# Optimization experiments

Hardware: AMD Instinct MI355X
Metric: run time of the kernel (lower is better)

## Reference

```python
import jax, jax.numpy as jnp
import numpy as np

B, T, E, H, OUT = 64, 2048, 512, 32, 131


def setup_inputs() -> dict:
    key = jax.random.key(0)
    ks = jax.random.split(key, 12)
    x = jax.random.normal(ks[0], (B, T, E), dtype=jnp.float32)
    # pack_padded_sequence(enforce_sorted=True) requires descending lengths
    src_len = jnp.sort(jax.random.randint(ks[1], (B,), 1, T + 1))[::-1]
    other_input = jax.random.normal(ks[2], (B, OUT), dtype=jnp.float32)
    s_ih, s_hh = 1.0 / np.sqrt(E), 1.0 / np.sqrt(H)
    W_ih_f = jax.random.normal(ks[3], (3 * H, E), dtype=jnp.float32) * s_ih
    W_hh_f = jax.random.normal(ks[4], (3 * H, H), dtype=jnp.float32) * s_hh
    b_ih_f = jax.random.normal(ks[5], (3 * H,), dtype=jnp.float32) * s_hh
    b_hh_f = jax.random.normal(ks[6], (3 * H,), dtype=jnp.float32) * s_hh
    W_ih_b = jax.random.normal(ks[7], (3 * H, E), dtype=jnp.float32) * s_ih
    W_hh_b = jax.random.normal(ks[8], (3 * H, H), dtype=jnp.float32) * s_hh
    b_ih_b = jax.random.normal(ks[9], (3 * H,), dtype=jnp.float32) * s_hh
    b_hh_b = jax.random.normal(ks[10], (3 * H,), dtype=jnp.float32) * s_hh
    fc_W = jax.random.normal(ks[11], (OUT, 2 * H), dtype=jnp.float32) * (1.0 / np.sqrt(2 * H))
    fc_b = jnp.zeros((OUT,), dtype=jnp.float32)
    return {"x": x, "src_len": src_len, "other_input": other_input,
            "W_ih_f": W_ih_f, "W_hh_f": W_hh_f, "b_ih_f": b_ih_f, "b_hh_f": b_hh_f,
            "W_ih_b": W_ih_b, "W_hh_b": W_hh_b, "b_ih_b": b_ih_b, "b_hh_b": b_hh_b,
            "fc_W": fc_W, "fc_b": fc_b}


def _gru_dir(x_proj, W_hh, b_hh, lengths, reverse):
    # x_proj: [B,T,3H] precomputed input gates; mask updates where t < length
    xs = jnp.swapaxes(x_proj, 0, 1)  # [T,B,3H]
    ts = jnp.arange(xs.shape[0])
    if reverse:
        xs, ts = xs[::-1], ts[::-1]

    def step(h, inp):
        gx, t = inp
        gh = h @ W_hh.T + b_hh
        xr, xz, xn = jnp.split(gx, 3, axis=-1)
        hr, hz, hn = jnp.split(gh, 3, axis=-1)
        r = jax.nn.sigmoid(xr + hr)
        z = jax.nn.sigmoid(xz + hz)
        n = jnp.tanh(xn + r * hn)
        h_new = (1.0 - z) * n + z * h
        mask = (t < lengths)[:, None]
        return jnp.where(mask, h_new, h), None

    h0 = jnp.zeros((x_proj.shape[0], W_hh.shape[1]), dtype=x_proj.dtype)
    h, _ = jax.lax.scan(step, h0, (xs, ts))
    return h  # [B,H] final hidden of this direction


def reference(x, src_len, other_input, W_ih_f, W_hh_f, b_ih_f, b_hh_f,
              W_ih_b, W_hh_b, b_ih_b, b_hh_b, fc_W, fc_b):
    lengths = src_len.astype(jnp.int32)
    # batched input projections (the only big GEMMs)
    xp_f = jnp.einsum('bte,ge->btg', x, W_ih_f) + b_ih_f  # [B,T,3H]
    xp_b = jnp.einsum('bte,ge->btg', x, W_ih_b) + b_ih_b
    h_f = _gru_dir(xp_f, W_hh_f, b_hh_f, lengths, reverse=False)
    h_b = _gru_dir(xp_b, W_hh_b, b_hh_b, lengths, reverse=True)
    # hidden_state[-2]=fwd, hidden_state[-1]=bwd for 1-layer bidirectional GRU
    hidden = jnp.concatenate([h_f, h_b], axis=1)  # [B,2H]
    return hidden @ fc_W.T + fc_b  # [B,OUT]
```

## Files before the change

kernel.cpp:

```cpp
#include <hip/hip_runtime.h>
#include <hip/hip_bf16.h>
#include <cstddef>
#include <cstdint>

typedef __bf16 bf16_t;
typedef __fp16 fp16_t;
typedef __attribute__((ext_vector_type(2))) __fp16 h16x2;
typedef __attribute__((ext_vector_type(8))) __bf16 bf16x8;
typedef __attribute__((ext_vector_type(4))) float f32x4;
typedef __attribute__((ext_vector_type(2))) unsigned u32x2;

#define B_  64
#define T_  2048
#define E_  512
#define H_  32
#define G_  96
#define N2_ 192
#define OUT_ 131

#define C1_ (-1.44269504088896340736f)
#define C2_ ( 2.88539008177792681472f)

#define MOVDPP(out_, in_, N_)                                               \
    asm("v_mov_b32_dpp %0, %1 row_ror:" #N_ " row_mask:0xf bank_mask:0xf"   \
        : "=v"(out_) : "v"(in_))

__global__ void prep_kernel(const float* __restrict__ Wf, const float* __restrict__ Wb,
                            const float* __restrict__ bf_, const float* __restrict__ bb_,
                            const float* __restrict__ bhf, const float* __restrict__ bhb,
                            bf16_t* __restrict__ Wbf, float* __restrict__ bias) {
    int idx = blockIdx.x * 256 + threadIdx.x;
    int g = idx >> 9, k = idx & 511;
    float v = (g < G_) ? Wf[g * E_ + k] : Wb[(g - G_) * E_ + k];
    Wbf[idx] = (bf16_t)v;
    if (idx < N2_) {
        int dn = (idx >= G_) ? 1 : 0;
        int lg = idx - G_ * dn;
        const float* bi = dn ? bb_ : bf_;
        const float* bh = dn ? bhb : bhf;
        bias[idx] = bi[lg] + ((lg < 64) ? bh[lg] : 0.0f);
    }
}

__global__ __launch_bounds__(256) void proj_kernel(
    const float* __restrict__ x,
    const bf16_t* __restrict__ Wbf,
    const float* __restrict__ bias,
    const int*   __restrict__ srcl,
    float* __restrict__ xp4)
{
    __shared__ bf16_t Alds[64][72];
    __shared__ bf16_t Blds[96][72];

    const int tid  = threadIdx.x;
    const int lane = tid & 63;
    const int w    = tid >> 6;
    const int wm   = w & 1;
    const int wn   = w >> 1;
    const int m0   = blockIdx.y * 64;
    const int n0   = blockIdx.x * 96;

    const int arow = tid >> 2;
    const int acol = (tid & 3) * 16;

    f32x4 acc[2][3];
    #pragma unroll
    for (int i = 0; i < 2; ++i)
        #pragma unroll
        for (int jn = 0; jn < 3; ++jn)
            acc[i][jn] = (f32x4){0.f, 0.f, 0.f, 0.f};

    for (int kt = 0; kt < 8; ++kt) {
        const int c0 = kt * 64;
        __syncthreads();
        {
            const float* asrc = x + (size_t)(m0 + arow) * E_ + c0 + acol;
            float4 v0 = *(const float4*)(asrc + 0);
            float4 v1 = *(const float4*)(asrc + 4);
            float4 v2 = *(const float4*)(asrc + 8);
            float4 v3 = *(const float4*)(asrc + 12);
            bf16x8 pa, pb;
            pa[0]=(bf16_t)v0.x; pa[1]=(bf16_t)v0.y; pa[2]=(bf16_t)v0.z; pa[3]=(bf16_t)v0.w;
            pa[4]=(bf16_t)v1.x; pa[5]=(bf16_t)v1.y; pa[6]=(bf16_t)v1.z; pa[7]=(bf16_t)v1.w;
            pb[0]=(bf16_t)v2.x; pb[1]=(bf16_t)v2.y; pb[2]=(bf16_t)v2.z; pb[3]=(bf16_t)v2.w;
            pb[4]=(bf16_t)v3.x; pb[5]=(bf16_t)v3.y; pb[6]=(bf16_t)v3.z; pb[7]=(bf16_t)v3.w;
            *(bf16x8*)&Alds[arow][acol]     = pa;
            *(bf16x8*)&Alds[arow][acol + 8] = pb;
        }
        #pragma unroll
        for (int i = 0; i < 3; ++i) {
            int u = tid + i * 256;
            int brow = u >> 3, koff = (u & 7) * 8;
            bf16x8 bv = *(const bf16x8*)(Wbf + (size_t)(n0 + brow) * E_ + c0 + koff);
            *(bf16x8*)&Blds[brow][koff] = bv;
        }
        __syncthreads();
        #pragma unroll
        for (int ks = 0; ks < 2; ++ks) {
            bf16x8 af[2], bfr[3];
            #pragma unroll
            for (int i = 0; i < 2; ++i)
                af[i] = *(const bf16x8*)&Alds[wm * 32 + i * 16 + (lane & 15)][ks * 32 + (lane >> 4) * 8];
            #pragma unroll
            for (int jn = 0; jn < 3; ++jn)
                bfr[jn] = *(const bf16x8*)&Blds[wn * 48 + jn * 16 + (lane & 15)][ks * 32 + (lane >> 4) * 8];
            #pragma unroll
            for (int i = 0; i < 2; ++i)
                #pragma unroll
                for (int jn = 0; jn < 3; ++jn)
                    acc[i][jn] = __builtin_amdgcn_mfma_f32_16x16x32_bf16(af[i], bfr[jn], acc[i][jn], 0, 0, 0);
        }
    }
    const int bb = m0 >> 11;
    int len = srcl[bb];
    if (len < 1) len = 1;
    if (len > T_) len = T_;
    float* xb4 = xp4 + (size_t)bb * 512 * N2_ * 4;
    #pragma unroll
    for (int i = 0; i < 2; ++i)
        #pragma unroll
        for (int jn = 0; jn < 3; ++jn) {
            int mg = m0 + wm * 32 + i * 16 + ((lane >> 4) & 3) * 4;
            int ng = n0 + wn * 48 + jn * 16 + (lane & 15);
            int lg = (ng >= G_) ? ng - G_ : ng;
            float scl = (lg < 64) ? C1_ : C2_;
            float bv  = bias[ng];
            int t = mg & (T_ - 1);
            if (ng < G_) {
                f32x4 v;
                #pragma unroll
                for (int r = 0; r < 4; ++r) v[r] = scl * (acc[i][jn][r] + bv);
                *(f32x4*)(xb4 + ((size_t)(t >> 2) * N2_ + ng) * 4) = v;
            } else {
                #pragma unroll
                for (int r = 0; r < 4; ++r) {
                    int trow = len - 1 - (t + r);
                    if (trow < 0) trow += T_;
                    xb4[((size_t)(trow >> 2) * N2_ + ng) * 4 + (trow & 3)] =
                        scl * (acc[i][jn][r] + bv);
                }
            }
        }
}

__global__ __launch_bounds__(64) void gru_rec_kernel(
    const float* __restrict__ xp4,
    const int*   __restrict__ src_len,
    const float* __restrict__ Whh_f, const float* __restrict__ bhh_f,
    const float* __restrict__ Whh_b, const float* __restrict__ bhh_b,
    float* __restrict__ hout)
{
    const int b    = blockIdx.x;
    const int l    = threadIdx.x;
    const int m    = l & 15;
    const int r16  = (l >> 4) & 1;
    const int dir  = l >> 5;
    const int j    = l & 31;

    const float* Whh = dir ? Whh_b : Whh_f;
    const float* bhh = dir ? bhh_b : bhh_f;

    int s_dir;
    {
        int q1;
        MOVDPP(q1, m, 1);
        s_dir = (__builtin_amdgcn_readfirstlane(q1) == 1) ? 1 : -1;
    }

    h16x2 wr[16], wz[16], wn[16];
    #pragma unroll
    for (int i = 0; i < 16; ++i) {
        int c  = (m + s_dir * i) & 15;
        int ka = c + 16 * r16;
        int kb = c + 16 * (1 - r16);
        wr[i] = (h16x2){(fp16_t)(C1_ * Whh[(j)      * H_ + ka]), (fp16_t)(C1_ * Whh[(j)      * H_ + kb])};
        wz[i] = (h16x2){(fp16_t)(C1_ * Whh[(32 + j) * H_ + ka]), (fp16_t)(C1_ * Whh[(32 + j) * H_ + kb])};
        wn[i] = (h16x2){(fp16_t)(C2_ * Whh[(64 + j) * H_ + ka]), (fp16_t)(C2_ * Whh[(64 + j) * H_ + kb])};
    }
    const float bn = C2_ * bhh[64 + j];

#if __has_builtin(__builtin_amdgcn_permlane16_swap)
    bool useX;
    {
        u32x2 pr = __builtin_amdgcn_permlane16_swap((unsigned)l, (unsigned)l, false, false);
        useX = (pr.x == (unsigned)(l ^ 16));
    }
#endif

    int len = src_len[b];
    if (len < 1) len = 1;
    if (len > T_) len = T_;
    len = __builtin_amdgcn_readfirstlane(len);

    const int off = dir * G_ + j;
    const float* xb4 = xp4 + (size_t)b * 512 * N2_ * 4;

    float hval = 0.0f;

    auto LB = [&](int q4, f32x4& vr, f32x4& vz, f32x4& vn) {
        int qq = (q4 < 512) ? q4 : 511;
        const f32x4* p = (const f32x4*)(xb4 + ((size_t)qq * N2_ + off) * 4);
        vr = p[0]; vz = p[32]; vn = p[64];
    };

    auto step = [&](float xr, float xz, float xn) {
        float hB;
#if __has_builtin(__builtin_amdgcn_permlane16_swap)
        {
            u32x2 sw = __builtin_amdgcn_permlane16_swap(
                __float_as_uint(hval), __float_as_uint(hval), false, false);
            hB = __uint_as_float(useX ? sw.x : sw.y);
        }
#else
        hB = __int_as_float(__builtin_amdgcn_ds_bpermute((l ^ 16) << 2, __float_as_int(hval)));
#endif
        auto q0 = __builtin_amdgcn_cvt_pkrtz(hval, hB);
        int qb = __builtin_bit_cast(int, q0);
        float ar = xr, az = xz, an = bn;
        {
            h16x2 p0 = __builtin_bit_cast(h16x2, qb);
            ar = __builtin_amdgcn_fdot2(p0, wr[0], ar, false);
            az = __builtin_amdgcn_fdot2(p0, wz[0], az, false);
            an = __builtin_amdgcn_fdot2(p0, wn[0], an, false);
        }
#define DOTI(N_)                                                    \
        {   int rb_;                                                \
            MOVDPP(rb_, qb, N_);                                    \
            h16x2 p_ = __builtin_bit_cast(h16x2, rb_);              \
            ar = __builtin_amdgcn_fdot2(p_, wr[N_], ar, false);     \
            az = __builtin_amdgcn_fdot2(p_, wz[N_], az, false);     \
            an = __builtin_amdgcn_fdot2(p_, wn[N_], an, false);     }
        DOTI(1)  DOTI(2)  DOTI(3)  DOTI(4)  DOTI(5)
        DOTI(6)  DOTI(7)  DOTI(8)  DOTI(9)  DOTI(10)
        DOTI(11) DOTI(12) DOTI(13) DOTI(14) DOTI(15)
#undef DOTI
        float er = __builtin_amdgcn_exp2f(ar);
        float rg = __builtin_amdgcn_rcpf(1.0f + er);
        float ez = __builtin_amdgcn_exp2f(az);
        float zg = __builtin_amdgcn_rcpf(1.0f + ez);
        float na = __builtin_fmaf(rg, an, xn);
        float eu = __builtin_amdgcn_exp2f(na);
        float u  = __builtin_amdgcn_rcpf(1.0f + eu);
        float m2 = -(ez + ez);
        float hp = hval + ez;
        hval = zg * __builtin_fmaf(m2, u, hp);
    };

    f32x4 Ar, Az, An, Cr, Cz, Cn;
    LB(0, Ar, Az, An);
    LB(1, Cr, Cz, Cn);
    int s = 0;
    while (s + 8 <= len) {
        step(Ar[0], Az[0], An[0]);
        step(Ar[1], Az[1], An[1]);
        step(Ar[2], Az[2], An[2]);
        step(Ar[3], Az[3], An[3]);
        LB((s >> 2) + 2, Ar, Az, An);
        step(Cr[0], Cz[0], Cn[0]);
        step(Cr[1], Cz[1], Cn[1]);
        step(Cr[2], Cz[2], Cn[2]);
        step(Cr[3], Cz[3], Cn[3]);
        LB((s >> 2) + 3, Cr, Cz, Cn);
        s += 8;
    }
    #pragma unroll
    for (int d = 0; d < 4; ++d)
        if (s + d < len) step(Ar[d], Az[d], An[d]);
    #pragma unroll
    for (int d = 0; d < 4; ++d)
        if (s + 4 + d < len) step(Cr[d], Cz[d], Cn[d]);

    hout[b * 64 + dir * 32 + j] = hval;
}

__global__ __launch_bounds__(192) void fc_kernel(
    const float* __restrict__ hbuf,
    const float* __restrict__ fcW,
    const float* __restrict__ fcb,
    float* __restrict__ out)
{
    __shared__ float hrow[64];
    const int b = blockIdx.x, tid = threadIdx.x;
    if (tid < 64) hrow[tid] = hbuf[b * 64 + tid];
    __syncthreads();
    if (tid < OUT_) {
        float acc = fcb[tid];
        #pragma unroll
        for (int i = 0; i < 64; ++i)
            acc = __builtin_fmaf(hrow[i], fcW[tid * 64 + i], acc);
        out[b * OUT_ + tid] = acc;
    }
}

extern "C" void kernel_launch(void* const* d_in, const int* in_sizes, int n_in,
                              void* d_out, int out_size, void* d_ws, size_t ws_size,
                              hipStream_t stream) {
    const float* x    = (const float*)d_in[0];
    const int*   srcl = (const int*)  d_in[1];
    const float* Wihf = (const float*)d_in[3];
    const float* Whhf = (const float*)d_in[4];
    const float* bihf = (const float*)d_in[5];
    const float* bhhf = (const float*)d_in[6];
    const float* Wihb = (const float*)d_in[7];
    const float* Whhb = (const float*)d_in[8];
    const float* bihb = (const float*)d_in[9];
    const float* bhhb = (const float*)d_in[10];
    const float* fcW  = (const float*)d_in[11];
    const float* fcb  = (const float*)d_in[12];
    float* out = (float*)d_out;

    const size_t XP_BYTES   = (size_t)B_ * T_ * N2_ * 4;
    const size_t HBUF_BYTES = (size_t)B_ * 64 * 4;
    const size_t BIAS_BYTES = 1024;
    const size_t WBF_BYTES  = (size_t)N2_ * E_ * 2;
    if (ws_size < XP_BYTES + HBUF_BYTES + BIAS_BYTES + WBF_BYTES) return;

    char* ws = (char*)d_ws;
    float*  xp4  = (float*)ws;
    float*  hbuf = (float*)(ws + XP_BYTES);
    float*  bias = (float*)(ws + XP_BYTES + HBUF_BYTES);
    bf16_t* Wbf  = (bf16_t*)(ws + XP_BYTES + HBUF_BYTES + BIAS_BYTES);

    prep_kernel<<<384, 256, 0, stream>>>(Wihf, Wihb, bihf, bihb, bhhf, bhhb, Wbf, bias);
    dim3 pg(2, (B_ * T_) / 64);
    proj_kernel<<<pg, 256, 0, stream>>>(x, Wbf, bias, srcl, xp4);
    gru_rec_kernel<<<B_, 64, 0, stream>>>(xp4, srcl, Whhf, bhhf, Whhb, bhhb, hbuf);
    fc_kernel<<<B_, 192, 0, stream>>>(hbuf, fcW, fcb, out);
}
```

Baseline: 454.8 us.

## Fuse projection GEMM and GRU recurrence with per-batch completion counters

```diff
diff --git a/kernel.cpp b/kernel.cpp
--- a/kernel.cpp
+++ b/kernel.cpp
@@ -28,7 +28,8 @@
 __global__ void prep_kernel(const float* __restrict__ Wf, const float* __restrict__ Wb,
                             const float* __restrict__ bf_, const float* __restrict__ bb_,
                             const float* __restrict__ bhf, const float* __restrict__ bhb,
-                            bf16_t* __restrict__ Wbf, float* __restrict__ bias) {
+                            bf16_t* __restrict__ Wbf, float* __restrict__ bias,
+                            int* __restrict__ done) {
     int idx = blockIdx.x * 256 + threadIdx.x;
     int g = idx >> 9, k = idx & 511;
     float v = (g < G_) ? Wf[g * E_ + k] : Wb[(g - G_) * E_ + k];
@@ -40,118 +41,129 @@
         const float* bh = dn ? bhb : bhf;
         bias[idx] = bi[lg] + ((lg < 64) ? bh[lg] : 0.0f);
     }
+    if (idx < B_) done[idx] = 0;
 }
 
-__global__ __launch_bounds__(256) void proj_kernel(
-    const float* __restrict__ x,
-    const bf16_t* __restrict__ Wbf,
-    const float* __restrict__ bias,
-    const int*   __restrict__ srcl,
-    float* __restrict__ xp4)
+__global__ __launch_bounds__(256) void fused_kernel(
+    const float* x,
+    const bf16_t* Wbf,
+    const float* bias,
+    const int* src_len,
+    const float* Whh_f, const float* bhh_f,
+    const float* Whh_b, const float* bhh_b,
+    float* xp4,
+    float* hout,
+    int* done)
 {
     __shared__ bf16_t Alds[64][72];
     __shared__ bf16_t Blds[96][72];
 
-    const int tid  = threadIdx.x;
-    const int lane = tid & 63;
-    const int w    = tid >> 6;
-    const int wm   = w & 1;
-    const int wn   = w >> 1;
-    const int m0   = blockIdx.y * 64;
-    const int n0   = blockIdx.x * 96;
-
-    const int arow = tid >> 2;
-    const int acol = (tid & 3) * 16;
-
-    f32x4 acc[2][3];
-    #pragma unroll
-    for (int i = 0; i < 2; ++i)
+    if (blockIdx.x >= 64) {
+        const int bx   = blockIdx.x - 64;
+        const int tid  = threadIdx.x;
+        const int lane = tid & 63;
+        const int w    = tid >> 6;
+        const int wm   = w & 1;
+        const int wn   = w >> 1;
+        const int m0   = (bx >> 1) * 64;
+        const int n0   = (bx & 1) * 96;
+
+        const int arow = tid >> 2;
+        const int acol = (tid & 3) * 16;
+
+        f32x4 acc[2][3];
         #pragma unroll
-        for (int jn = 0; jn < 3; ++jn)
-            acc[i][jn] = (f32x4){0.f, 0.f, 0.f, 0.f};
-
-    for (int kt = 0; kt < 8; ++kt) {
-        const int c0 = kt * 64;
-        __syncthreads();
-        {
-            const float* asrc = x + (size_t)(m0 + arow) * E_ + c0 + acol;
-            float4 v0 = *(const float4*)(asrc + 0);
-            float4 v1 = *(const float4*)(asrc + 4);
-            float4 v2 = *(const float4*)(asrc + 8);
-            float4 v3 = *(const float4*)(asrc + 12);
-            bf16x8 pa, pb;
-            pa[0]=(bf16_t)v0.x; pa[1]=(bf16_t)v0.y; pa[2]=(bf16_t)v0.z; pa[3]=(bf16_t)v0.w;
-            pa[4]=(bf16_t)v1.x; pa[5]=(bf16_t)v1.y; pa[6]=(bf16_t)v1.z; pa[7]=(bf16_t)v1.w;
-            pb[0]=(bf16_t)v2.x; pb[1]=(bf16_t)v2.y; pb[2]=(bf16_t)v2.z; pb[3]=(bf16_t)v2.w;
-            pb[4]=(bf16_t)v3.x; pb[5]=(bf16_t)v3.y; pb[6]=(bf16_t)v3.z; pb[7]=(bf16_t)v3.w;
-            *(bf16x8*)&Alds[arow][acol]     = pa;
-            *(bf16x8*)&Alds[arow][acol + 8] = pb;
-        }
-        #pragma unroll
-        for (int i = 0; i < 3; ++i) {
-            int u = tid + i * 256;
-            int brow = u >> 3, koff = (u & 7) * 8;
-            bf16x8 bv = *(const bf16x8*)(Wbf + (size_t)(n0 + brow) * E_ + c0 + koff);
-            *(bf16x8*)&Blds[brow][koff] = bv;
-        }
-        __syncthreads();
-        #pragma unroll
-        for (int ks = 0; ks < 2; ++ks) {
-            bf16x8 af[2], bfr[3];
-            #pragma unroll
-            for (int i = 0; i < 2; ++i)
-                af[i] = *(const bf16x8*)&Alds[wm * 32 + i * 16 + (lane & 15)][ks * 32 + (lane >> 4) * 8];
+        for (int i = 0; i < 2; ++i)
             #pragma unroll
             for (int jn = 0; jn < 3; ++jn)
-                bfr[jn] = *(const bf16x8*)&Blds[wn * 48 + jn * 16 + (lane & 15)][ks * 32 + (lane >> 4) * 8];
+                acc[i][jn] = (f32x4){0.f, 0.f, 0.f, 0.f};
+
+        for (int kt = 0; kt < 8; ++kt) {
+            const int c0 = kt * 64;
+            __syncthreads();
+            {
+                const float* asrc = x + (size_t)(m0 + arow) * E_ + c0 + acol;
+                float4 v0 = *(const float4*)(asrc + 0);
+                float4 v1 = *(const float4*)(asrc + 4);
+                float4 v2 = *(const float4*)(asrc + 8);
+                float4 v3 = *(const float4*)(asrc + 12);
+                bf16x8 pa, pb;
+                pa[0]=(bf16_t)v0.x; pa[1]=(bf16_t)v0.y; pa[2]=(bf16_t)v0.z; pa[3]=(bf16_t)v0.w;
+                pa[4]=(bf16_t)v1.x; pa[5]=(bf16_t)v1.y; pa[6]=(bf16_t)v1.z; pa[7]=(bf16_t)v1.w;
+                pb[0]=(bf16_t)v2.x; pb[1]=(bf16_t)v2.y; pb[2]=(bf16_t)v2.z; pb[3]=(bf16_t)v2.w;
+                pb[4]=(bf16_t)v3.x; pb[5]=(bf16_t)v3.y; pb[6]=(bf16_t)v3.z; pb[7]=(bf16_t)v3.w;
+                *(bf16x8*)&Alds[arow][acol]     = pa;
+                *(bf16x8*)&Alds[arow][acol + 8] = pb;
+            }
             #pragma unroll
-            for (int i = 0; i < 2; ++i)
+            for (int i = 0; i < 3; ++i) {
+                int u = tid + i * 256;
+                int brow = u >> 3, koff = (u & 7) * 8;
+                bf16x8 bv = *(const bf16x8*)(Wbf + (size_t)(n0 + brow) * E_ + c0 + koff);
+                *(bf16x8*)&Blds[brow][koff] = bv;
+            }
+            __syncthreads();
+            #pragma unroll
+            for (int ks = 0; ks < 2; ++ks) {
+                bf16x8 af[2], bfr[3];
+                #pragma unroll
+                for (int i = 0; i < 2; ++i)
+                    af[i] = *(const bf16x8*)&Alds[wm * 32 + i * 16 + (lane & 15)][ks * 32 + (lane >> 4) * 8];
                 #pragma unroll
                 for (int jn = 0; jn < 3; ++jn)
-                    acc[i][jn] = __builtin_amdgcn_mfma_f32_16x16x32_bf16(af[i], bfr[jn], acc[i][jn], 0, 0, 0);
+                    bfr[jn] = *(const bf16x8*)&Blds[wn * 48 + jn * 16 + (lane & 15)][ks * 32 + (lane >> 4) * 8];
+                #pragma unroll
+                for (int i = 0; i < 2; ++i)
+                    #pragma unroll
+                    for (int jn = 0; jn < 3; ++jn)
+                        acc[i][jn] = __builtin_amdgcn_mfma_f32_16x16x32_bf16(af[i], bfr[jn], acc[i][jn], 0, 0, 0);
+            }
         }
-    }
-    const int bb = m0 >> 11;
-    int len = srcl[bb];
-    if (len < 1) len = 1;
-    if (len > T_) len = T_;
-    float* xb4 = xp4 + (size_t)bb * 512 * N2_ * 4;
-    #pragma unroll
-    for (int i = 0; i < 2; ++i)
+        const int bb = m0 >> 11;
+        int len = src_len[bb];
+        if (len < 1) len = 1;
+        if (len > T_) len = T_;
+        float* xb4 = xp4 + (size_t)bb * 512 * N2_ * 4;
         #pragma unroll
-        for (int jn = 0; jn < 3; ++jn) {
-            int mg = m0 + wm * 32 + i * 16 + ((lane >> 4) & 3) * 4;
-            int ng = n0 + wn * 48 + jn * 16 + (lane & 15);
-            int lg = (ng >= G_) ? ng - G_ : ng;
-            float scl = (lg < 64) ? C1_ : C2_;
-            float bv  = bias[ng];
-            int t = mg & (T_ - 1);
-            if (ng < G_) {
-                f32x4 v;
-                #pragma unroll
-                for (int r = 0; r < 4; ++r) v[r] = scl * (acc[i][jn][r] + bv);
-                *(f32x4*)(xb4 + ((size_t)(t >> 2) * N2_ + ng) * 4) = v;
-            } else {
-                #pragma unroll
-                for (int r = 0; r < 4; ++r) {
-                    int trow = len - 1 - (t + r);
-                    if (trow < 0) trow += T_;
-                    xb4[((size_t)(trow >> 2) * N2_ + ng) * 4 + (trow & 3)] =
-                        scl * (acc[i][jn][r] + bv);
+        for (int i = 0; i < 2; ++i)
+            #pragma unroll
+            for (int jn = 0; jn < 3; ++jn) {
+                int mg = m0 + wm * 32 + i * 16 + ((lane >> 4) & 3) * 4;
+                int ng = n0 + wn * 48 + jn * 16 + (lane & 15);
+                int lg = (ng >= G_) ? ng - G_ : ng;
+                float scl = (lg < 64) ? C1_ : C2_;
+                float bv  = bias[ng];
+                int t = mg & (T_ - 1);
+                if (ng < G_) {
+                    f32x4 v;
+                    #pragma unroll
+                    for (int r = 0; r < 4; ++r) v[r] = scl * (acc[i][jn][r] + bv);
+                    *(f32x4*)(xb4 + ((size_t)(t >> 2) * N2_ + ng) * 4) = v;
+                } else {
+                    #pragma unroll
+                    for (int r = 0; r < 4; ++r) {
+                        int trow = len - 1 - (t + r);
+                        if (trow < 0) trow += T_;
+                        xb4[((size_t)(trow >> 2) * N2_ + ng) * 4 + (trow & 3)] =
+                            scl * (acc[i][jn][r] + bv);
+                    }
                 }
             }
-        }
-}
-
-__global__ __launch_bounds__(64) void gru_rec_kernel(
-    const float* __restrict__ xp4,
-    const int*   __restrict__ src_len,
-    const float* __restrict__ Whh_f, const float* __restrict__ bhh_f,
-    const float* __restrict__ Whh_b, const float* __restrict__ bhh_b,
-    float* __restrict__ hout)
-{
-    const int b    = blockIdx.x;
-    const int l    = threadIdx.x;
+        __threadfence();
+        __syncthreads();
+        if (tid == 0) atomicAdd(&done[bb], 1);
+        return;
+    }
+
+    const int b = blockIdx.x;
+    const int l = threadIdx.x;
+    if (l >= 64) return;
+
+    if (l == 0) {
+        while (atomicAdd(&done[b], 0) < 64) {}
+    }
+    __threadfence();
+
     const int m    = l & 15;
     const int r16  = (l >> 4) & 1;
     const int dir  = l >> 5;
@@ -313,17 +325,18 @@
     const size_t HBUF_BYTES = (size_t)B_ * 64 * 4;
     const size_t BIAS_BYTES = 1024;
     const size_t WBF_BYTES  = (size_t)N2_ * E_ * 2;
-    if (ws_size < XP_BYTES + HBUF_BYTES + BIAS_BYTES + WBF_BYTES) return;
+    const size_t DONE_BYTES = 256;
+    if (ws_size < XP_BYTES + HBUF_BYTES + BIAS_BYTES + WBF_BYTES + DONE_BYTES) return;
 
     char* ws = (char*)d_ws;
     float*  xp4  = (float*)ws;
     float*  hbuf = (float*)(ws + XP_BYTES);
     float*  bias = (float*)(ws + XP_BYTES + HBUF_BYTES);
     bf16_t* Wbf  = (bf16_t*)(ws + XP_BYTES + HBUF_BYTES + BIAS_BYTES);
-
-    prep_kernel<<<384, 256, 0, stream>>>(Wihf, Wihb, bihf, bihb, bhhf, bhhb, Wbf, bias);
-    dim3 pg(2, (B_ * T_) / 64);
-    proj_kernel<<<pg, 256, 0, stream>>>(x, Wbf, bias, srcl, xp4);
-    gru_rec_kernel<<<B_, 64, 0, stream>>>(xp4, srcl, Whhf, bhhf, Whhb, bhhb, hbuf);
+    int*    done = (int*)(ws + XP_BYTES + HBUF_BYTES + BIAS_BYTES + WBF_BYTES);
+
+    prep_kernel<<<384, 256, 0, stream>>>(Wihf, Wihb, bihf, bihb, bhhf, bhhb, Wbf, bias, done);
+    fused_kernel<<<64 + (B_ * T_) / 64 * 2, 256, 0, stream>>>(
+        x, Wbf, bias, srcl, Whhf, bhhf, Whhb, bhhb, xp4, hbuf, done);
     fc_kernel<<<B_, 192, 0, stream>>>(hbuf, fcW, fcb, out);
 }
```

Result: slower. 1.045 ms (+129.7%).

## Split GRU recurrence across two half-waves per direction with permlane32 reduction

Applied to the files above, without the earlier changes.

```diff
diff --git a/kernel.cpp b/kernel.cpp
--- a/kernel.cpp
+++ b/kernel.cpp
@@ -21,9 +21,13 @@
 #define C1_ (-1.44269504088896340736f)
 #define C2_ ( 2.88539008177792681472f)
 
-#define MOVDPP(out_, in_, N_)                                               \
-    asm("v_mov_b32_dpp %0, %1 row_ror:" #N_ " row_mask:0xf bank_mask:0xf"   \
-        : "=v"(out_) : "v"(in_))
+#if __has_builtin(__builtin_amdgcn_mov_dpp)
+#define DPPROT(out_, in_, N_) (out_) = __builtin_amdgcn_mov_dpp((in_), 0x120 + (N_), 0xf, 0xf, false)
+#else
+#define DPPROT(out_, in_, N_)                                               \
+    asm("s_nop 1\n\ts_nop 1\n\tv_mov_b32_dpp %0, %1 row_ror:" #N_           \
+        " row_mask:0xf bank_mask:0xf" : "=v"(out_) : "v"(in_))
+#endif
 
 __global__ void prep_kernel(const float* __restrict__ Wf, const float* __restrict__ Wb,
                             const float* __restrict__ bf_, const float* __restrict__ bb_,
@@ -150,11 +154,13 @@
     const float* __restrict__ Whh_b, const float* __restrict__ bhh_b,
     float* __restrict__ hout)
 {
-    const int b    = blockIdx.x;
+    const int blk  = blockIdx.x;
+    const int b    = blk >> 1;
+    const int dir  = blk & 1;
     const int l    = threadIdx.x;
     const int m    = l & 15;
     const int r16  = (l >> 4) & 1;
-    const int dir  = l >> 5;
+    const int p32  = l >> 5;
     const int j    = l & 31;
 
     const float* Whh = dir ? Whh_b : Whh_f;
@@ -163,21 +169,21 @@
     int s_dir;
     {
         int q1;
-        MOVDPP(q1, m, 1);
+        DPPROT(q1, m, 1);
         s_dir = (__builtin_amdgcn_readfirstlane(q1) == 1) ? 1 : -1;
     }
 
-    h16x2 wr[16], wz[16], wn[16];
-    #pragma unroll
-    for (int i = 0; i < 16; ++i) {
-        int c  = (m + s_dir * i) & 15;
+    h16x2 wr[8], wz[8], wn[8];
+    #pragma unroll
+    for (int i = 0; i < 8; ++i) {
+        int c  = (m + s_dir * (i + 8 * p32)) & 15;
         int ka = c + 16 * r16;
         int kb = c + 16 * (1 - r16);
         wr[i] = (h16x2){(fp16_t)(C1_ * Whh[(j)      * H_ + ka]), (fp16_t)(C1_ * Whh[(j)      * H_ + kb])};
         wz[i] = (h16x2){(fp16_t)(C1_ * Whh[(32 + j) * H_ + ka]), (fp16_t)(C1_ * Whh[(32 + j) * H_ + kb])};
         wn[i] = (h16x2){(fp16_t)(C2_ * Whh[(64 + j) * H_ + ka]), (fp16_t)(C2_ * Whh[(64 + j) * H_ + kb])};
     }
-    const float bn = C2_ * bhh[64 + j];
+    const float bnseed = p32 ? 0.0f : (C2_ * bhh[64 + j]);
 
 #if __has_builtin(__builtin_amdgcn_permlane16_swap)
     bool useX;
@@ -199,8 +205,17 @@
 
     auto LB = [&](int q4, f32x4& vr, f32x4& vz, f32x4& vn) {
         int qq = (q4 < 512) ? q4 : 511;
-        const f32x4* p = (const f32x4*)(xb4 + ((size_t)qq * N2_ + off) * 4);
-        vr = p[0]; vz = p[32]; vn = p[64];
+        const f32x4* pp = (const f32x4*)(xb4 + ((size_t)qq * N2_ + off) * 4);
+        vr = pp[0]; vz = pp[32]; vn = pp[64];
+    };
+
+    auto pl32sum = [&](float a) -> float {
+#if __has_builtin(__builtin_amdgcn_permlane32_swap)
+        u32x2 rr = __builtin_amdgcn_permlane32_swap(__float_as_uint(a), __float_as_uint(a), false, false);
+        return __uint_as_float(rr.x) + __uint_as_float(rr.y);
+#else
+        return a + __int_as_float(__builtin_amdgcn_ds_bpermute((l ^ 32) << 2, __float_as_int(a)));
+#endif
     };
 
     auto step = [&](float xr, float xz, float xn) {
@@ -216,29 +231,33 @@
 #endif
         auto q0 = __builtin_amdgcn_cvt_pkrtz(hval, hB);
         int qb = __builtin_bit_cast(int, q0);
-        float ar = xr, az = xz, an = bn;
+        int qb8;
+        DPPROT(qb8, qb, 8);
+        int qc = p32 ? qb8 : qb;
+        float ar = 0.f, az = 0.f, an = bnseed;
         {
-            h16x2 p0 = __builtin_bit_cast(h16x2, qb);
-            ar = __builtin_amdgcn_fdot2(p0, wr[0], ar, false);
-            az = __builtin_amdgcn_fdot2(p0, wz[0], az, false);
-            an = __builtin_amdgcn_fdot2(p0, wn[0], an, false);
+            h16x2 p_ = __builtin_bit_cast(h16x2, qc);
+            ar = __builtin_amdgcn_fdot2(p_, wr[0], ar, false);
+            az = __builtin_amdgcn_fdot2(p_, wz[0], az, false);
+            an = __builtin_amdgcn_fdot2(p_, wn[0], an, false);
         }
 #define DOTI(N_)                                                    \
         {   int rb_;                                                \
-            MOVDPP(rb_, qb, N_);                                    \
+            DPPROT(rb_, qc, N_);                                    \
             h16x2 p_ = __builtin_bit_cast(h16x2, rb_);              \
             ar = __builtin_amdgcn_fdot2(p_, wr[N_], ar, false);     \
             az = __builtin_amdgcn_fdot2(p_, wz[N_], az, false);     \
             an = __builtin_amdgcn_fdot2(p_, wn[N_], an, false);     }
-        DOTI(1)  DOTI(2)  DOTI(3)  DOTI(4)  DOTI(5)
-        DOTI(6)  DOTI(7)  DOTI(8)  DOTI(9)  DOTI(10)
-        DOTI(11) DOTI(12) DOTI(13) DOTI(14) DOTI(15)
+        DOTI(1) DOTI(2) DOTI(3) DOTI(4) DOTI(5) DOTI(6) DOTI(7)
 #undef DOTI
-        float er = __builtin_amdgcn_exp2f(ar);
+        float arf = pl32sum(ar) + xr;
+        float azf = pl32sum(az) + xz;
+        float anf = pl32sum(an);
+        float er = __builtin_amdgcn_exp2f(arf);
         float rg = __builtin_amdgcn_rcpf(1.0f + er);
-        float ez = __builtin_amdgcn_exp2f(az);
+        float ez = __builtin_amdgcn_exp2f(azf);
         float zg = __builtin_amdgcn_rcpf(1.0f + ez);
-        float na = __builtin_fmaf(rg, an, xn);
+        float na = __builtin_fmaf(rg, anf, xn);
         float eu = __builtin_amdgcn_exp2f(na);
         float u  = __builtin_amdgcn_rcpf(1.0f + eu);
         float m2 = -(ez + ez);
@@ -270,7 +289,7 @@
     for (int d = 0; d < 4; ++d)
         if (s + 4 + d < len) step(Cr[d], Cz[d], Cn[d]);
 
-    hout[b * 64 + dir * 32 + j] = hval;
+    if (p32 == 0) hout[b * 64 + dir * 32 + j] = hval;
 }
 
 __global__ __launch_bounds__(192) void fc_kernel(
@@ -324,6 +343,6 @@
     prep_kernel<<<384, 256, 0, stream>>>(Wihf, Wihb, bihf, bihb, bhhf, bhhb, Wbf, bias);
     dim3 pg(2, (B_ * T_) / 64);
     proj_kernel<<<pg, 256, 0, stream>>>(x, Wbf, bias, srcl, xp4);
-    gru_rec_kernel<<<B_, 64, 0, stream>>>(xp4, srcl, Whhf, bhhf, Whhb, bhhb, hbuf);
+    gru_rec_kernel<<<B_ * 2, 64, 0, stream>>>(xp4, srcl, Whhf, bhhf, Whhb, bhhb, hbuf);
     fc_kernel<<<B_, 192, 0, stream>>>(hbuf, fcW, fcb, out);
 }
```

Result: no change. 462.9 us (+1.8%).
